# Optimization experiments

Measured on AMD Instinct MI355X. Metric: run time of the kernel, lower is better.

The kernel has to match this reference:

```python
import jax, jax.numpy as jnp
import numpy as np
from jax import lax

C = 256
B, H, W = 8, 64, 64


def dwconv(x, w, b, pad):
    # x: [B,C,H,W], w: [C,1,kh,kw] depthwise (groups=C), b: [C]
    y = lax.conv_general_dilated(
        x, w,
        window_strides=(1, 1),
        padding=pad,
        dimension_numbers=('NCHW', 'OIHW', 'NCHW'),
        feature_group_count=x.shape[1],
    )
    return y + b[None, :, None, None]


def setup_inputs() -> dict:
    key = jax.random.key(0)
    ks = jax.random.split(key, 16)
    s = 0.05
    inp = {
        'x': jax.random.normal(ks[0], (B, C, H, W), jnp.float32),
        'w0':   jax.random.normal(ks[1], (C, 1, 5, 5), jnp.float32) * s,
        'b0':   jax.random.normal(ks[2], (C,), jnp.float32) * s,
        'w0_1': jax.random.normal(ks[3], (C, 1, 1, 7), jnp.float32) * s,
        'b0_1': jax.random.normal(ks[4], (C,), jnp.float32) * s,
        'w0_2': jax.random.normal(ks[5], (C, 1, 7, 1), jnp.float32) * s,
        'b0_2': jax.random.normal(ks[6], (C,), jnp.float32) * s,
        'w1_1': jax.random.normal(ks[7], (C, 1, 1, 11), jnp.float32) * s,
        'b1_1': jax.random.normal(ks[8], (C,), jnp.float32) * s,
        'w1_2': jax.random.normal(ks[9], (C, 1, 11, 1), jnp.float32) * s,
        'b1_2': jax.random.normal(ks[10], (C,), jnp.float32) * s,
        'w2_1': jax.random.normal(ks[11], (C, 1, 1, 21), jnp.float32) * s,
        'b2_1': jax.random.normal(ks[12], (C,), jnp.float32) * s,
        'w2_2': jax.random.normal(ks[13], (C, 1, 21, 1), jnp.float32) * s,
        'b2_2': jax.random.normal(ks[14], (C,), jnp.float32) * s,
    }
    return inp


def reference(x, w0, b0, w0_1, b0_1, w0_2, b0_2,
              w1_1, b1_1, w1_2, b1_2, w2_1, b2_1, w2_2, b2_2):
    # 5x5 depthwise, pad 2
    attn = dwconv(x, w0, b0, ((2, 2), (2, 2)))
    # stage 0: 1x7 / 7x1 strips
    a0x = dwconv(attn, w0_1, b0_1, ((0, 0), (3, 3)))
    a0y = dwconv(attn, w0_2, b0_2, ((3, 3), (0, 0)))
    attn_0 = a0x * a0y
    # stage 1: 1x11 / 11x1 strips
    a1x = dwconv(a0x, w1_1, b1_1, ((0, 0), (5, 5)))
    a1y = dwconv(a0y, w1_2, b1_2, ((5, 5), (0, 0)))
    attn_1 = a1x * a1y
    # stage 2: 1x21 / 21x1 strips
    a2x = dwconv(a1x, w2_1, b2_1, ((0, 0), (10, 10)))
    a2y = dwconv(a1y, w2_2, b2_2, ((10, 10), (0, 0)))
    attn_2 = a2x * a2y
    return (attn_0, attn_1, attn_2)
```

## Files before the change

kernel.cpp:

```cpp
#include <hip/hip_runtime.h>


#define RW 4352
#define LDS_WORDS (4 * RW)

typedef float v2f __attribute__((ext_vector_type(2)));

__device__ __forceinline__ float dppsr1(float v) {
    return __int_as_float(__builtin_amdgcn_update_dpp(
        0, __float_as_int(v), 0x111, 0xF, 0xF, false));
}
__device__ __forceinline__ float dppsr2(float v) {
    return __int_as_float(__builtin_amdgcn_update_dpp(
        0, __float_as_int(v), 0x112, 0xF, 0xF, false));
}
__device__ __forceinline__ float dppsl1(float v) {
    return __int_as_float(__builtin_amdgcn_update_dpp(
        0, __float_as_int(v), 0x101, 0xF, 0xF, false));
}
__device__ __forceinline__ float dppsl2(float v) {
    return __int_as_float(__builtin_amdgcn_update_dpp(
        0, __float_as_int(v), 0x102, 0xF, 0xF, false));
}
__device__ __forceinline__ void ld8(const float* p, float* d) {
    float4 a = *(const float4*)p, b = *(const float4*)(p + 4);
    d[0]=a.x; d[1]=a.y; d[2]=a.z; d[3]=a.w; d[4]=b.x; d[5]=b.y; d[6]=b.z; d[7]=b.w;
}
__device__ __forceinline__ void ld4p(const float* p, v2f* w) {
    float4 q = *(const float4*)p;
    w[0].x = q.x; w[0].y = q.y; w[1].x = q.z; w[1].y = q.w;
}
__device__ __forceinline__ void st4p(float* p, v2f a, v2f b) {
    float4 q; q.x = a.x; q.y = a.y; q.z = b.x; q.w = b.y;
    *(float4*)p = q;
}
__device__ __forceinline__ float elem(const v2f* a, int e) {
    return (e & 1) ? a[e >> 1].y : a[e >> 1].x;
}

template<int K, int TAPOFF, int NP>
__device__ __forceinline__ void conv_acc(const float* __restrict__ wrow,
                                         const v2f* wnd, v2f* A) {
    #pragma unroll
    for (int v = 0; v < K; v++) {
        const float w = wrow[v];
        const int u = v + TAPOFF;
        if ((u & 1) == 0) {
            v2f wv; wv.x = w; wv.y = w;
            #pragma unroll
            for (int k = 0; k < NP; k++) A[k] += wv * wnd[(u >> 1) + k];
        } else {
            #pragma unroll
            for (int k = 0; k < NP; k++) {
                A[k].x += w * wnd[(u >> 1) + k].y;
                A[k].y += w * wnd[(u >> 1) + k + 1].x;
            }
        }
    }
}

template<int H>
__device__ __forceinline__ void sconv_pk(const float* __restrict__ wt, float bb,
                                         const v2f* a, bool pm, bool np, v2f* acc) {
    constexpr int HE = H + 1;
    float pe[HE], ne[HE];
    pe[0] = 0.f;
    #pragma unroll
    for (int i = 1; i < HE; i++) {
        float tmp = dppsr1(elem(a, 8 - HE + i));
        pe[i] = pm ? tmp : 0.f;
    }
    #pragma unroll
    for (int i = 0; i < H; i++) {
        float tmp = dppsl1(elem(a, i));
        ne[i] = np ? tmp : 0.f;
    }
    ne[H] = 0.f;
    v2f wnd[HE + 4];
    #pragma unroll
    for (int m = 0; m < HE / 2; m++) { wnd[m].x = pe[2 * m]; wnd[m].y = pe[2 * m + 1]; }
    #pragma unroll
    for (int k = 0; k < 4; k++) wnd[HE / 2 + k] = a[k];
    #pragma unroll
    for (int m = 0; m < HE / 2; m++) {
        wnd[HE / 2 + 4 + m].x = ne[2 * m]; wnd[HE / 2 + 4 + m].y = ne[2 * m + 1];
    }
    #pragma unroll
    for (int k = 0; k < 4; k++) { acc[k].x = bb; acc[k].y = bb; }
    conv_acc<2 * H + 1, 1, 4>(wt, wnd, acc);
}

__device__ __forceinline__ void sconv21_pk(const float* __restrict__ wt, float bb,
                                           const v2f* a, bool pm, bool pm2,
                                           bool np, bool np2, v2f* acc) {
    float pe[10], ne[10];
    { float t0 = dppsr2(elem(a, 6)); pe[0] = pm2 ? t0 : 0.f; }
    { float t1 = dppsr2(elem(a, 7)); pe[1] = pm2 ? t1 : 0.f; }
    #pragma unroll
    for (int i = 0; i < 8; i++) {
        float tmp = dppsr1(elem(a, i));
        pe[2 + i] = pm ? tmp : 0.f;
    }
    #pragma unroll
    for (int i = 0; i < 8; i++) {
        float tmp = dppsl1(elem(a, i));
        ne[i] = np ? tmp : 0.f;
    }
    { float t0 = dppsl2(elem(a, 0)); ne[8] = np2 ? t0 : 0.f; }
    { float t1 = dppsl2(elem(a, 1)); ne[9] = np2 ? t1 : 0.f; }
    v2f wnd[14];
    #pragma unroll
    for (int m = 0; m < 5; m++) { wnd[m].x = pe[2 * m]; wnd[m].y = pe[2 * m + 1]; }
    #pragma unroll
    for (int k = 0; k < 4; k++) wnd[5 + k] = a[k];
    #pragma unroll
    for (int m = 0; m < 5; m++) { wnd[9 + m].x = ne[2 * m]; wnd[9 + m].y = ne[2 * m + 1]; }
    #pragma unroll
    for (int k = 0; k < 4; k++) { acc[k].x = bb; acc[k].y = bb; }
    conv_acc<21, 0, 4>(wt, wnd, acc);
}

__global__ __launch_bounds__(512, 4)
void msca_fused(const float* __restrict__ x,
                const float* __restrict__ w0,   const float* __restrict__ b0,
                const float* __restrict__ w0_1, const float* __restrict__ b0_1,
                const float* __restrict__ w0_2, const float* __restrict__ b0_2,
                const float* __restrict__ w1_1, const float* __restrict__ b1_1,
                const float* __restrict__ w1_2, const float* __restrict__ b1_2,
                const float* __restrict__ w2_1, const float* __restrict__ b2_1,
                const float* __restrict__ w2_2, const float* __restrict__ b2_2,
                float* __restrict__ out)
{
    __shared__ __align__(16) float lds[LDS_WORDS];
    float* RT = lds;
    float* R0 = lds + RW;
    float* R1 = lds + 2 * RW;
    float* R2 = lds + 3 * RW;

    const int t     = threadIdx.x;
    const int maj   = t >> 3;
    const int lane8 = t & 7;
    const int j0    = lane8 << 3;

    const bool pm  = lane8 >= 1, np  = lane8 <= 6;
    const bool pm2 = lane8 >= 2, np2 = lane8 <= 5;

    const int scat = maj ^ (lane8 << 3);
    const int rdb  = maj * 68 + ((lane8 ^ ((maj >> 3) & 7)) << 3);

    const int plane = blockIdx.x;
    const int ch    = plane & 255;

    const float* xg = x + (size_t)plane * 4096;
    float* o0 = out + (size_t)plane * 4096;
    float* o1 = o0 + 8388608;
    float* o2 = o1 + 8388608;

    v2f attn[4];
    {
        const float bb = b0[ch];
        #pragma unroll
        for (int k = 0; k < 4; k++) { attn[k].x = bb; attn[k].y = bb; }
        const float* w0p = w0 + ch * 25;
        #pragma unroll
        for (int dr = 0; dr < 5; dr++) {
            const int ri = maj + dr - 2;
            const int rc = ri < 0 ? 0 : (ri > 63 ? 63 : ri);
            const bool valid = (unsigned)ri <= 63u;
            float a[8];
            ld8(&xg[rc * 64 + j0], a);
            #pragma unroll
            for (int i = 0; i < 8; i++) a[i] = valid ? a[i] : 0.f;
            float l0 = dppsr1(a[6]), l1 = dppsr1(a[7]);
            float r0 = dppsl1(a[0]), r1 = dppsl1(a[1]);
            v2f wnd[6];
            wnd[0].x = pm ? l0 : 0.f;  wnd[0].y = pm ? l1 : 0.f;
            wnd[1].x = a[0]; wnd[1].y = a[1];
            wnd[2].x = a[2]; wnd[2].y = a[3];
            wnd[3].x = a[4]; wnd[3].y = a[5];
            wnd[4].x = a[6]; wnd[4].y = a[7];
            wnd[5].x = np ? r0 : 0.f;  wnd[5].y = np ? r1 : 0.f;
            conv_acc<5, 0, 4>(w0p + dr * 5, wnd, attn);
        }
        #pragma unroll
        for (int e = 0; e < 8; e++) RT[(j0 + e) * 68 + scat] = elem(attn, e);
    }
    __syncthreads();

    v2f a0x[4], a1x[4], a2x[4];
    {
        v2f stv[4];
        ld4p(&RT[rdb],     &stv[0]);
        ld4p(&RT[rdb + 4], &stv[2]);

        v2f a0y[4];
        sconv_pk<3>(w0_2 + ch * 7, b0_2[ch], stv, pm, np, a0y);
        #pragma unroll
        for (int d = 0; d < 8; d++) R0[(j0 + d) * 68 + scat] = elem(a0y, d);
        sconv_pk<3>(w0_1 + ch * 7, b0_1[ch], attn, pm, np, a0x);

        v2f a1y[4];
        sconv_pk<5>(w1_2 + ch * 11, b1_2[ch], a0y, pm, np, a1y);
        #pragma unroll
        for (int d = 0; d < 8; d++) R1[(j0 + d) * 68 + scat] = elem(a1y, d);
        sconv_pk<5>(w1_1 + ch * 11, b1_1[ch], a0x, pm, np, a1x);

        v2f a2y[4];
        sconv21_pk(w2_2 + ch * 21, b2_2[ch], a1y, pm, pm2, np, np2, a2y);
        #pragma unroll
        for (int d = 0; d < 8; d++) R2[(j0 + d) * 68 + scat] = elem(a2y, d);
        sconv21_pk(w2_1 + ch * 21, b2_1[ch], a1x, pm, pm2, np, np2, a2x);
    }
    __syncthreads();

    {
        v2f y0r[4], y1r[4], y2r[4];
        ld4p(&R0[rdb],     &y0r[0]);
        ld4p(&R0[rdb + 4], &y0r[2]);
        ld4p(&R1[rdb],     &y1r[0]);
        ld4p(&R1[rdb + 4], &y1r[2]);
        ld4p(&R2[rdb],     &y2r[0]);
        ld4p(&R2[rdb + 4], &y2r[2]);
        {
            v2f q0 = a0x[0] * y0r[0], q1 = a0x[1] * y0r[1];
            v2f q2 = a0x[2] * y0r[2], q3 = a0x[3] * y0r[3];
            st4p(&o0[maj * 64 + j0],     q0, q1);
            st4p(&o0[maj * 64 + j0 + 4], q2, q3);
        }
        {
            v2f q0 = a1x[0] * y1r[0], q1 = a1x[1] * y1r[1];
            v2f q2 = a1x[2] * y1r[2], q3 = a1x[3] * y1r[3];
            st4p(&o1[maj * 64 + j0],     q0, q1);
            st4p(&o1[maj * 64 + j0 + 4], q2, q3);
        }
        {
            v2f q0 = a2x[0] * y2r[0], q1 = a2x[1] * y2r[1];
            v2f q2 = a2x[2] * y2r[2], q3 = a2x[3] * y2r[3];
            st4p(&o2[maj * 64 + j0],     q0, q1);
            st4p(&o2[maj * 64 + j0 + 4], q2, q3);
        }
    }
}

extern "C" void kernel_launch(void* const* d_in, const int* in_sizes, int n_in,
                              void* d_out, int out_size, void* d_ws, size_t ws_size,
                              hipStream_t stream) {
    msca_fused<<<2048, 512, 0, stream>>>(
        (const float*)d_in[0],
        (const float*)d_in[1],  (const float*)d_in[2],
        (const float*)d_in[3],  (const float*)d_in[4],
        (const float*)d_in[5],  (const float*)d_in[6],
        (const float*)d_in[7],  (const float*)d_in[8],
        (const float*)d_in[9],  (const float*)d_in[10],
        (const float*)d_in[11], (const float*)d_in[12],
        (const float*)d_in[13], (const float*)d_in[14],
        (float*)d_out);
}
```

Baseline: 43.02 us.

## Use 1024 threads per plane with 4 pixels per thread and deferred x-branch

Switches from 512 threads handling 8 pixels each to 1024 threads handling 4 pixels each. Each row is now spread over 16 lanes, so neighbour exchange uses DPP shifts of up to 3 lanes. The horizontal strip convolutions are moved after the second barrier to cut live registers. The aim is more parallelism and lower register pressure per thread, at the cost of more halo DPP traffic and redundant edge work per pixel.

```diff
diff --git a/kernel.cpp b/kernel.cpp
--- a/kernel.cpp
+++ b/kernel.cpp
@@ -6,26 +6,12 @@
 
 typedef float v2f __attribute__((ext_vector_type(2)));
 
-__device__ __forceinline__ float dppsr1(float v) {
+template<int C>
+__device__ __forceinline__ float dpp(float v) {
     return __int_as_float(__builtin_amdgcn_update_dpp(
-        0, __float_as_int(v), 0x111, 0xF, 0xF, false));
-}
-__device__ __forceinline__ float dppsr2(float v) {
-    return __int_as_float(__builtin_amdgcn_update_dpp(
-        0, __float_as_int(v), 0x112, 0xF, 0xF, false));
-}
-__device__ __forceinline__ float dppsl1(float v) {
-    return __int_as_float(__builtin_amdgcn_update_dpp(
-        0, __float_as_int(v), 0x101, 0xF, 0xF, false));
-}
-__device__ __forceinline__ float dppsl2(float v) {
-    return __int_as_float(__builtin_amdgcn_update_dpp(
-        0, __float_as_int(v), 0x102, 0xF, 0xF, false));
-}
-__device__ __forceinline__ void ld8(const float* p, float* d) {
-    float4 a = *(const float4*)p, b = *(const float4*)(p + 4);
-    d[0]=a.x; d[1]=a.y; d[2]=a.z; d[3]=a.w; d[4]=b.x; d[5]=b.y; d[6]=b.z; d[7]=b.w;
-}
+        0, __float_as_int(v), C, 0xF, 0xF, false));
+}
+
 __device__ __forceinline__ void ld4p(const float* p, v2f* w) {
     float4 q = *(const float4*)p;
     w[0].x = q.x; w[0].y = q.y; w[1].x = q.z; w[1].y = q.w;
@@ -59,68 +45,89 @@
     }
 }
 
-template<int H>
-__device__ __forceinline__ void sconv_pk(const float* __restrict__ wt, float bb,
-                                         const v2f* a, bool pm, bool np, v2f* acc) {
-    constexpr int HE = H + 1;
-    float pe[HE], ne[HE];
-    pe[0] = 0.f;
-    #pragma unroll
-    for (int i = 1; i < HE; i++) {
-        float tmp = dppsr1(elem(a, 8 - HE + i));
-        pe[i] = pm ? tmp : 0.f;
-    }
-    #pragma unroll
-    for (int i = 0; i < H; i++) {
-        float tmp = dppsl1(elem(a, i));
-        ne[i] = np ? tmp : 0.f;
-    }
-    ne[H] = 0.f;
-    v2f wnd[HE + 4];
-    #pragma unroll
-    for (int m = 0; m < HE / 2; m++) { wnd[m].x = pe[2 * m]; wnd[m].y = pe[2 * m + 1]; }
-    #pragma unroll
-    for (int k = 0; k < 4; k++) wnd[HE / 2 + k] = a[k];
-    #pragma unroll
-    for (int m = 0; m < HE / 2; m++) {
-        wnd[HE / 2 + 4 + m].x = ne[2 * m]; wnd[HE / 2 + 4 + m].y = ne[2 * m + 1];
-    }
-    #pragma unroll
-    for (int k = 0; k < 4; k++) { acc[k].x = bb; acc[k].y = bb; }
-    conv_acc<2 * H + 1, 1, 4>(wt, wnd, acc);
-}
-
-__device__ __forceinline__ void sconv21_pk(const float* __restrict__ wt, float bb,
-                                           const v2f* a, bool pm, bool pm2,
-                                           bool np, bool np2, v2f* acc) {
-    float pe[10], ne[10];
-    { float t0 = dppsr2(elem(a, 6)); pe[0] = pm2 ? t0 : 0.f; }
-    { float t1 = dppsr2(elem(a, 7)); pe[1] = pm2 ? t1 : 0.f; }
-    #pragma unroll
-    for (int i = 0; i < 8; i++) {
-        float tmp = dppsr1(elem(a, i));
-        pe[2 + i] = pm ? tmp : 0.f;
-    }
-    #pragma unroll
-    for (int i = 0; i < 8; i++) {
-        float tmp = dppsl1(elem(a, i));
-        ne[i] = np ? tmp : 0.f;
-    }
-    { float t0 = dppsl2(elem(a, 0)); ne[8] = np2 ? t0 : 0.f; }
-    { float t1 = dppsl2(elem(a, 1)); ne[9] = np2 ? t1 : 0.f; }
-    v2f wnd[14];
-    #pragma unroll
-    for (int m = 0; m < 5; m++) { wnd[m].x = pe[2 * m]; wnd[m].y = pe[2 * m + 1]; }
-    #pragma unroll
-    for (int k = 0; k < 4; k++) wnd[5 + k] = a[k];
-    #pragma unroll
-    for (int m = 0; m < 5; m++) { wnd[9 + m].x = ne[2 * m]; wnd[9 + m].y = ne[2 * m + 1]; }
-    #pragma unroll
-    for (int k = 0; k < 4; k++) { acc[k].x = bb; acc[k].y = bb; }
-    conv_acc<21, 0, 4>(wt, wnd, acc);
-}
-
-__global__ __launch_bounds__(512, 4)
+__device__ __forceinline__ void sconv7(const float* __restrict__ wt, float bb,
+                                       const v2f* a, bool pm1, bool np1, v2f* acc) {
+    float p1 = dpp<0x111>(a[0].y);
+    float p2 = dpp<0x111>(a[1].x);
+    float p3 = dpp<0x111>(a[1].y);
+    float n0 = dpp<0x101>(a[0].x);
+    float n1 = dpp<0x101>(a[0].y);
+    float n2 = dpp<0x101>(a[1].x);
+    v2f wnd[6];
+    wnd[0].x = 0.f;              wnd[0].y = pm1 ? p1 : 0.f;
+    wnd[1].x = pm1 ? p2 : 0.f;   wnd[1].y = pm1 ? p3 : 0.f;
+    wnd[2] = a[0]; wnd[3] = a[1];
+    wnd[4].x = np1 ? n0 : 0.f;   wnd[4].y = np1 ? n1 : 0.f;
+    wnd[5].x = np1 ? n2 : 0.f;   wnd[5].y = 0.f;
+    acc[0].x = bb; acc[0].y = bb; acc[1].x = bb; acc[1].y = bb;
+    conv_acc<7, 1, 2>(wt, wnd, acc);
+}
+
+__device__ __forceinline__ void sconv11(const float* __restrict__ wt, float bb,
+                                        const v2f* a, bool pm1, bool pm2,
+                                        bool np1, bool np2, v2f* acc) {
+    float q3 = dpp<0x112>(a[1].y);
+    float p0 = dpp<0x111>(a[0].x);
+    float p1 = dpp<0x111>(a[0].y);
+    float p2 = dpp<0x111>(a[1].x);
+    float p3 = dpp<0x111>(a[1].y);
+    float n0 = dpp<0x101>(a[0].x);
+    float n1 = dpp<0x101>(a[0].y);
+    float n2 = dpp<0x101>(a[1].x);
+    float n3 = dpp<0x101>(a[1].y);
+    float m0 = dpp<0x102>(a[0].x);
+    v2f wnd[8];
+    wnd[0].x = 0.f;             wnd[0].y = pm2 ? q3 : 0.f;
+    wnd[1].x = pm1 ? p0 : 0.f;  wnd[1].y = pm1 ? p1 : 0.f;
+    wnd[2].x = pm1 ? p2 : 0.f;  wnd[2].y = pm1 ? p3 : 0.f;
+    wnd[3] = a[0]; wnd[4] = a[1];
+    wnd[5].x = np1 ? n0 : 0.f;  wnd[5].y = np1 ? n1 : 0.f;
+    wnd[6].x = np1 ? n2 : 0.f;  wnd[6].y = np1 ? n3 : 0.f;
+    wnd[7].x = np2 ? m0 : 0.f;  wnd[7].y = 0.f;
+    acc[0].x = bb; acc[0].y = bb; acc[1].x = bb; acc[1].y = bb;
+    conv_acc<11, 1, 2>(wt, wnd, acc);
+}
+
+__device__ __forceinline__ void sconv21(const float* __restrict__ wt, float bb,
+                                        const v2f* a, bool pm1, bool pm2, bool pm3,
+                                        bool np1, bool np2, bool np3, v2f* acc) {
+    float s32 = dpp<0x113>(a[1].x);
+    float s33 = dpp<0x113>(a[1].y);
+    float s20 = dpp<0x112>(a[0].x);
+    float s21 = dpp<0x112>(a[0].y);
+    float s22 = dpp<0x112>(a[1].x);
+    float s23 = dpp<0x112>(a[1].y);
+    float s10 = dpp<0x111>(a[0].x);
+    float s11 = dpp<0x111>(a[0].y);
+    float s12 = dpp<0x111>(a[1].x);
+    float s13 = dpp<0x111>(a[1].y);
+    float t10 = dpp<0x101>(a[0].x);
+    float t11 = dpp<0x101>(a[0].y);
+    float t12 = dpp<0x101>(a[1].x);
+    float t13 = dpp<0x101>(a[1].y);
+    float t20 = dpp<0x102>(a[0].x);
+    float t21 = dpp<0x102>(a[0].y);
+    float t22 = dpp<0x102>(a[1].x);
+    float t23 = dpp<0x102>(a[1].y);
+    float t30 = dpp<0x103>(a[0].x);
+    float t31 = dpp<0x103>(a[0].y);
+    v2f wnd[12];
+    wnd[0].x  = pm3 ? s32 : 0.f;  wnd[0].y  = pm3 ? s33 : 0.f;
+    wnd[1].x  = pm2 ? s20 : 0.f;  wnd[1].y  = pm2 ? s21 : 0.f;
+    wnd[2].x  = pm2 ? s22 : 0.f;  wnd[2].y  = pm2 ? s23 : 0.f;
+    wnd[3].x  = pm1 ? s10 : 0.f;  wnd[3].y  = pm1 ? s11 : 0.f;
+    wnd[4].x  = pm1 ? s12 : 0.f;  wnd[4].y  = pm1 ? s13 : 0.f;
+    wnd[5] = a[0]; wnd[6] = a[1];
+    wnd[7].x  = np1 ? t10 : 0.f;  wnd[7].y  = np1 ? t11 : 0.f;
+    wnd[8].x  = np1 ? t12 : 0.f;  wnd[8].y  = np1 ? t13 : 0.f;
+    wnd[9].x  = np2 ? t20 : 0.f;  wnd[9].y  = np2 ? t21 : 0.f;
+    wnd[10].x = np2 ? t22 : 0.f;  wnd[10].y = np2 ? t23 : 0.f;
+    wnd[11].x = np3 ? t30 : 0.f;  wnd[11].y = np3 ? t31 : 0.f;
+    acc[0].x = bb; acc[0].y = bb; acc[1].x = bb; acc[1].y = bb;
+    conv_acc<21, 0, 2>(wt, wnd, acc);
+}
+
+__global__ __launch_bounds__(1024, 8)
 void msca_fused(const float* __restrict__ x,
                 const float* __restrict__ w0,   const float* __restrict__ b0,
                 const float* __restrict__ w0_1, const float* __restrict__ b0_1,
@@ -137,16 +144,16 @@
     float* R1 = lds + 2 * RW;
     float* R2 = lds + 3 * RW;
 
-    const int t     = threadIdx.x;
-    const int maj   = t >> 3;
-    const int lane8 = t & 7;
-    const int j0    = lane8 << 3;
-
-    const bool pm  = lane8 >= 1, np  = lane8 <= 6;
-    const bool pm2 = lane8 >= 2, np2 = lane8 <= 5;
-
-    const int scat = maj ^ (lane8 << 3);
-    const int rdb  = maj * 68 + ((lane8 ^ ((maj >> 3) & 7)) << 3);
+    const int t   = threadIdx.x;
+    const int maj = t >> 4;
+    const int l16 = t & 15;
+    const int j0  = l16 << 2;
+
+    const bool pm1 = l16 >= 1, pm2 = l16 >= 2, pm3 = l16 >= 3;
+    const bool np1 = l16 <= 14, np2 = l16 <= 13, np3 = l16 <= 12;
+
+    const int scat = maj ^ (l16 << 2);
+    const int rdb  = maj * 68 + ((l16 ^ ((maj >> 2) & 15)) << 2);
 
     const int plane = blockIdx.x;
     const int ch    = plane & 255;
@@ -156,96 +163,76 @@
     float* o1 = o0 + 8388608;
     float* o2 = o1 + 8388608;
 
-    v2f attn[4];
+    v2f attn[2];
     {
         const float bb = b0[ch];
-        #pragma unroll
-        for (int k = 0; k < 4; k++) { attn[k].x = bb; attn[k].y = bb; }
+        attn[0].x = bb; attn[0].y = bb; attn[1].x = bb; attn[1].y = bb;
         const float* w0p = w0 + ch * 25;
         #pragma unroll
         for (int dr = 0; dr < 5; dr++) {
             const int ri = maj + dr - 2;
             const int rc = ri < 0 ? 0 : (ri > 63 ? 63 : ri);
             const bool valid = (unsigned)ri <= 63u;
-            float a[8];
-            ld8(&xg[rc * 64 + j0], a);
-            #pragma unroll
-            for (int i = 0; i < 8; i++) a[i] = valid ? a[i] : 0.f;
-            float l0 = dppsr1(a[6]), l1 = dppsr1(a[7]);
-            float r0 = dppsl1(a[0]), r1 = dppsl1(a[1]);
-            v2f wnd[6];
-            wnd[0].x = pm ? l0 : 0.f;  wnd[0].y = pm ? l1 : 0.f;
-            wnd[1].x = a[0]; wnd[1].y = a[1];
-            wnd[2].x = a[2]; wnd[2].y = a[3];
-            wnd[3].x = a[4]; wnd[3].y = a[5];
-            wnd[4].x = a[6]; wnd[4].y = a[7];
-            wnd[5].x = np ? r0 : 0.f;  wnd[5].y = np ? r1 : 0.f;
-            conv_acc<5, 0, 4>(w0p + dr * 5, wnd, attn);
+            float4 q = *(const float4*)&xg[rc * 64 + j0];
+            float a0 = valid ? q.x : 0.f, a1 = valid ? q.y : 0.f;
+            float a2 = valid ? q.z : 0.f, a3 = valid ? q.w : 0.f;
+            float L0 = dpp<0x111>(a2), L1 = dpp<0x111>(a3);
+            float Rr0 = dpp<0x101>(a0), Rr1 = dpp<0x101>(a1);
+            v2f wnd[4];
+            wnd[0].x = pm1 ? L0 : 0.f;   wnd[0].y = pm1 ? L1 : 0.f;
+            wnd[1].x = a0; wnd[1].y = a1;
+            wnd[2].x = a2; wnd[2].y = a3;
+            wnd[3].x = np1 ? Rr0 : 0.f;  wnd[3].y = np1 ? Rr1 : 0.f;
+            conv_acc<5, 0, 2>(w0p + dr * 5, wnd, attn);
         }
         #pragma unroll
-        for (int e = 0; e < 8; e++) RT[(j0 + e) * 68 + scat] = elem(attn, e);
+        for (int e = 0; e < 4; e++) RT[(j0 + e) * 68 + scat] = elem(attn, e);
     }
     __syncthreads();
 
-    v2f a0x[4], a1x[4], a2x[4];
     {
-        v2f stv[4];
-        ld4p(&RT[rdb],     &stv[0]);
-        ld4p(&RT[rdb + 4], &stv[2]);
-
-        v2f a0y[4];
-        sconv_pk<3>(w0_2 + ch * 7, b0_2[ch], stv, pm, np, a0y);
-        #pragma unroll
-        for (int d = 0; d < 8; d++) R0[(j0 + d) * 68 + scat] = elem(a0y, d);
-        sconv_pk<3>(w0_1 + ch * 7, b0_1[ch], attn, pm, np, a0x);
-
-        v2f a1y[4];
-        sconv_pk<5>(w1_2 + ch * 11, b1_2[ch], a0y, pm, np, a1y);
-        #pragma unroll
-        for (int d = 0; d < 8; d++) R1[(j0 + d) * 68 + scat] = elem(a1y, d);
-        sconv_pk<5>(w1_1 + ch * 11, b1_1[ch], a0x, pm, np, a1x);
-
-        v2f a2y[4];
-        sconv21_pk(w2_2 + ch * 21, b2_2[ch], a1y, pm, pm2, np, np2, a2y);
-        #pragma unroll
-        for (int d = 0; d < 8; d++) R2[(j0 + d) * 68 + scat] = elem(a2y, d);
-        sconv21_pk(w2_1 + ch * 21, b2_1[ch], a1x, pm, pm2, np, np2, a2x);
+        v2f stv[2];
+        ld4p(&RT[rdb], stv);
+        v2f a0y[2];
+        sconv7(w0_2 + ch * 7, b0_2[ch], stv, pm1, np1, a0y);
+        #pragma unroll
+        for (int d = 0; d < 4; d++) R0[(j0 + d) * 68 + scat] = elem(a0y, d);
+        v2f a1y[2];
+        sconv11(w1_2 + ch * 11, b1_2[ch], a0y, pm1, pm2, np1, np2, a1y);
+        #pragma unroll
+        for (int d = 0; d < 4; d++) R1[(j0 + d) * 68 + scat] = elem(a1y, d);
+        v2f a2y[2];
+        sconv21(w2_2 + ch * 21, b2_2[ch], a1y, pm1, pm2, pm3, np1, np2, np3, a2y);
+        #pragma unroll
+        for (int d = 0; d < 4; d++) R2[(j0 + d) * 68 + scat] = elem(a2y, d);
     }
     __syncthreads();
 
     {
-        v2f y0r[4], y1r[4], y2r[4];
-        ld4p(&R0[rdb],     &y0r[0]);
-        ld4p(&R0[rdb + 4], &y0r[2]);
-        ld4p(&R1[rdb],     &y1r[0]);
-        ld4p(&R1[rdb + 4], &y1r[2]);
-        ld4p(&R2[rdb],     &y2r[0]);
-        ld4p(&R2[rdb + 4], &y2r[2]);
-        {
-            v2f q0 = a0x[0] * y0r[0], q1 = a0x[1] * y0r[1];
-            v2f q2 = a0x[2] * y0r[2], q3 = a0x[3] * y0r[3];
-            st4p(&o0[maj * 64 + j0],     q0, q1);
-            st4p(&o0[maj * 64 + j0 + 4], q2, q3);
-        }
-        {
-            v2f q0 = a1x[0] * y1r[0], q1 = a1x[1] * y1r[1];
-            v2f q2 = a1x[2] * y1r[2], q3 = a1x[3] * y1r[3];
-            st4p(&o1[maj * 64 + j0],     q0, q1);
-            st4p(&o1[maj * 64 + j0 + 4], q2, q3);
-        }
-        {
-            v2f q0 = a2x[0] * y2r[0], q1 = a2x[1] * y2r[1];
-            v2f q2 = a2x[2] * y2r[2], q3 = a2x[3] * y2r[3];
-            st4p(&o2[maj * 64 + j0],     q0, q1);
-            st4p(&o2[maj * 64 + j0 + 4], q2, q3);
-        }
+        v2f y0r[2];
+        ld4p(&R0[rdb], y0r);
+        v2f a0x[2];
+        sconv7(w0_1 + ch * 7, b0_1[ch], attn, pm1, np1, a0x);
+        st4p(&o0[maj * 64 + j0], a0x[0] * y0r[0], a0x[1] * y0r[1]);
+
+        v2f y1r[2];
+        ld4p(&R1[rdb], y1r);
+        v2f a1x[2];
+        sconv11(w1_1 + ch * 11, b1_1[ch], a0x, pm1, pm2, np1, np2, a1x);
+        st4p(&o1[maj * 64 + j0], a1x[0] * y1r[0], a1x[1] * y1r[1]);
+
+        v2f y2r[2];
+        ld4p(&R2[rdb], y2r);
+        v2f a2x[2];
+        sconv21(w2_1 + ch * 21, b2_1[ch], a1x, pm1, pm2, pm3, np1, np2, np3, a2x);
+        st4p(&o2[maj * 64 + j0], a2x[0] * y2r[0], a2x[1] * y2r[1]);
     }
 }
 
 extern "C" void kernel_launch(void* const* d_in, const int* in_sizes, int n_in,
                               void* d_out, int out_size, void* d_ws, size_t ws_size,
                               hipStream_t stream) {
-    msca_fused<<<2048, 512, 0, stream>>>(
+    msca_fused<<<2048, 1024, 0, stream>>>(
         (const float*)d_in[0],
         (const float*)d_in[1],  (const float*)d_in[2],
         (const float*)d_in[3],  (const float*)d_in[4],
```

Result: no change. 42.30 us (-1.7%).
